# Kernel optimization log

Measured on AMD Instinct MI355X. Metric: run time of the kernel, lower is better.

## Reference

```python
import jax, jax.numpy as jnp
import numpy as np

DIM, ATT, G, T, KL, B = 1024, 128, 8, 4096, 256, 8
GD = DIM // G
SCALE = 1.0 / np.sqrt(ATT)

def setup_inputs() -> dict:
    key = jax.random.key(0)
    ks = jax.random.split(key, 7)
    x = jax.random.normal(ks[0], (B, T, DIM), dtype=jnp.float32)
    # stacked per-group weights (einsum orientation: in_dim x out_dim)
    Wq = jax.random.normal(ks[1], (G, GD, ATT), dtype=jnp.float32) * (1.0 / np.sqrt(GD))
    Wk = jax.random.normal(ks[2], (G, GD, ATT), dtype=jnp.float32) * (1.0 / np.sqrt(GD))
    Wv = jax.random.normal(ks[3], (G, GD, GD), dtype=jnp.float32) * (1.0 / np.sqrt(GD))
    Wo = jax.random.normal(ks[4], (G, GD, GD), dtype=jnp.float32) * (1.0 / np.sqrt(GD))
    Pk = jax.random.normal(ks[5], (G, T, KL), dtype=jnp.float32) * (1.0 / np.sqrt(T))
    Pv = jax.random.normal(ks[6], (G, T, KL), dtype=jnp.float32) * (1.0 / np.sqrt(T))
    return {"x": x, "Wq": Wq, "Wk": Wk, "Wv": Wv, "Wo": Wo, "Pk": Pk, "Pv": Pv}

def reference(x, Wq, Wk, Wv, Wo, Pk, Pv):
    Bx, Tx, _ = x.shape
    xg = x.reshape(Bx, Tx, G, GD).transpose(0, 2, 1, 3)        # [B,G,T,gd]
    q = jnp.einsum('bgtd,gda->bgta', xg, Wq)                   # [B,G,T,att]
    k = jnp.einsum('bgtd,gda->bgta', xg, Wk)
    v = jnp.einsum('bgtd,gde->bgte', xg, Wv)                   # [B,G,T,gd]
    k_red = jnp.einsum('bgta,gtk->bgka', k, Pk)                # [B,G,kl,att]
    v_red = jnp.einsum('bgte,gtk->bgke', v, Pv)                # [B,G,kl,gd]
    att = jax.nn.softmax(jnp.einsum('bgta,bgka->bgtk', q, k_red) * SCALE, axis=-1)
    out = jnp.einsum('bgtk,bgke->bgte', att, v_red)            # [B,G,T,gd]
    out = jnp.einsum('bgte,gef->bgtf', out, Wo)                # per-group output proj
    return out.transpose(0, 2, 1, 3).reshape(Bx, Tx, DIM)      # concat groups on last dim
```

## Files before the change

kernel.cpp:

```cpp
#include <hip/hip_runtime.h>
#include <hip/hip_bf16.h>

#define NB 8
#define NG 8
#define NT 4096
#define NDIM 1024
#define NGD 128
#define NATT 128
#define NKL 256
#define FSCALE 0.08838834764831845f

typedef __bf16 bf16x8 __attribute__((ext_vector_type(8)));
typedef float f32x4 __attribute__((ext_vector_type(4)));
typedef ushort u16x8 __attribute__((ext_vector_type(8)));
typedef ushort u16x4 __attribute__((ext_vector_type(4)));

#define MFMA(a, b, c) __builtin_amdgcn_mfma_f32_16x16x32_bf16(a, b, c, 0, 0, 0)

__device__ __forceinline__ ushort f2bf(float f) {
  union { float f; unsigned u; } v; v.f = f;
  unsigned r = v.u + 0x7FFFu + ((v.u >> 16) & 1u);
  return (ushort)(r >> 16);
}

__device__ __forceinline__ void gload16(const ushort* g, ushort* l) {
  __builtin_amdgcn_global_load_lds(
      (const __attribute__((address_space(1))) unsigned int*)g,
      (__attribute__((address_space(3))) unsigned int*)l, 16, 0, 0);
}

__global__ __launch_bounds__(512) void k0_weights(
    const float* __restrict__ Wq, const float* __restrict__ Wk,
    const float* __restrict__ Wv, const float* __restrict__ Wo,
    ushort* __restrict__ WkQT, ushort* __restrict__ WvoT) {
  const int sel = blockIdx.x;
  const int g = blockIdx.y;
  __shared__ float A2[128 * 136];
  __shared__ float B2[128 * 136];
  const int tid = threadIdx.x;

  if (sel == 0) {
#pragma unroll
    for (int u = 0; u < 8; ++u) {
      const int c = tid + 512 * u;
      const int row = c >> 5, c4 = (c & 31) * 4;
      *(float4*)&A2[row * 136 + c4] =
          *(const float4*)&Wo[(size_t)g * 16384 + row * 128 + c4];
      const float4 v = *(const float4*)&Wv[(size_t)g * 16384 + row * 128 + c4];
      B2[(c4 + 0) * 136 + row] = v.x;
      B2[(c4 + 1) * 136 + row] = v.y;
      B2[(c4 + 2) * 136 + row] = v.z;
      B2[(c4 + 3) * 136 + row] = v.w;
    }
  } else {
#pragma unroll
    for (int u = 0; u < 8; ++u) {
      const int c = tid + 512 * u;
      const int row = c >> 5, c4 = (c & 31) * 4;
      const float4 q = *(const float4*)&Wq[(size_t)g * 16384 + row * 128 + c4];
      A2[(c4 + 0) * 136 + row] = q.x;
      A2[(c4 + 1) * 136 + row] = q.y;
      A2[(c4 + 2) * 136 + row] = q.z;
      A2[(c4 + 3) * 136 + row] = q.w;
      const float4 k = *(const float4*)&Wk[(size_t)g * 16384 + row * 128 + c4];
      B2[(c4 + 0) * 136 + row] = k.x;
      B2[(c4 + 1) * 136 + row] = k.y;
      B2[(c4 + 2) * 136 + row] = k.z;
      B2[(c4 + 3) * 136 + row] = k.w;
    }
  }
  __syncthreads();

  const int mr = tid >> 4;
  const int mc = tid & 15;
  float acc[4][8];
#pragma unroll
  for (int i = 0; i < 4; ++i)
#pragma unroll
    for (int j = 0; j < 8; ++j) acc[i][j] = 0.f;

#pragma unroll 4
  for (int k = 0; k < 128; ++k) {
    const float4 a = *(const float4*)&A2[k * 136 + mr * 4];
    const float4 b0 = *(const float4*)&B2[k * 136 + mc * 8];
    const float4 b1 = *(const float4*)&B2[k * 136 + mc * 8 + 4];
    const float av[4] = {a.x, a.y, a.z, a.w};
    const float bv[8] = {b0.x, b0.y, b0.z, b0.w, b1.x, b1.y, b1.z, b1.w};
#pragma unroll
    for (int i = 0; i < 4; ++i)
#pragma unroll
      for (int j = 0; j < 8; ++j) acc[i][j] += av[i] * bv[j];
  }

  const float sc = sel ? FSCALE : 1.f;
  ushort* dst = (sel ? WkQT : WvoT) + (size_t)g * 16384;
#pragma unroll
  for (int i = 0; i < 4; ++i) {
    u16x8 pk;
#pragma unroll
    for (int j = 0; j < 8; ++j) pk[j] = f2bf(acc[i][j] * sc);
    *(u16x8*)&dst[(size_t)(mr * 4 + i) * 128 + mc * 8] = pk;
  }
}

__global__ __launch_bounds__(256) void kt_x(const float* __restrict__ x,
                                            ushort* __restrict__ xT) {
  const int t0 = blockIdx.x * 64;
  const int bg = blockIdx.y;
  const int b = bg >> 3, g = bg & 7;
  __shared__ float xl[64 * 132];
#pragma unroll
  for (int u = 0; u < 8; ++u) {
    const int c = threadIdx.x + 256 * u;
    const int row = c >> 5, c4 = (c & 31) * 4;
    *(float4*)&xl[row * 132 + c4] =
        *(const float4*)&x[((size_t)b * NT + t0 + row) * NDIM + g * 128 + c4];
  }
  __syncthreads();
  const int d = threadIdx.x >> 1, th = (threadIdx.x & 1) * 32;
  ushort* dst = xT + ((size_t)bg * 128 + d) * NT + t0 + th;
#pragma unroll
  for (int k = 0; k < 8; ++k) {
    u16x4 pk;
#pragma unroll
    for (int z = 0; z < 4; ++z) pk[z] = f2bf(xl[(th + k * 4 + z) * 132 + d]);
    *(u16x4*)&dst[k * 4] = pk;
  }
}

__global__ __launch_bounds__(256) void kt_p(const float* __restrict__ P,
                                            ushort* __restrict__ PT) {
  const int t0 = blockIdx.x * 64;
  const int klh = blockIdx.y, g = blockIdx.z;
  __shared__ float pl[64 * 132];
#pragma unroll
  for (int u = 0; u < 8; ++u) {
    const int c = threadIdx.x + 256 * u;
    const int row = c >> 5, c4 = (c & 31) * 4;
    *(float4*)&pl[row * 132 + c4] =
        *(const float4*)&P[((size_t)g * NT + t0 + row) * NKL + klh * 128 + c4];
  }
  __syncthreads();
  const int d = threadIdx.x >> 1, th = (threadIdx.x & 1) * 32;
  ushort* dst = PT + ((size_t)g * NKL + klh * 128 + d) * NT + t0 + th;
#pragma unroll
  for (int k = 0; k < 8; ++k) {
    u16x4 pk;
#pragma unroll
    for (int z = 0; z < 4; ++z) pk[z] = f2bf(pl[(th + k * 4 + z) * 132 + d]);
    *(u16x4*)&dst[k * 4] = pk;
  }
}

__global__ __launch_bounds__(256, 2) void k1_mfma(
    const ushort* __restrict__ PkT, const ushort* __restrict__ PvT,
    const ushort* __restrict__ xT, const ushort* __restrict__ WkQT,
    const ushort* __restrict__ WvoT, ushort* __restrict__ MQ,
    ushort* __restrict__ vo_redT) {
  const int klt = blockIdx.x;
  const int sel = blockIdx.y;
  const int bg = blockIdx.z;
  const int g = bg & 7;
  const ushort* PT = (sel ? PvT : PkT) + ((size_t)g * NKL + klt * 128) * NT;
  const ushort* Xb = xT + (size_t)bg * 128 * NT;

  __shared__ ushort lds[17408];

  const int tid = threadIdx.x;
  const int w = tid >> 6, lane = tid & 63;
  const int l15 = lane & 15, l4 = lane >> 4;
  const int rh = (w & 1) * 64;
  const int ch = (w >> 1) * 64;
  const int srow = lane >> 2, sc = lane & 3;

  f32x4 acc[4][4];
  const f32x4 fz = {0.f, 0.f, 0.f, 0.f};
#pragma unroll
  for (int i = 0; i < 4; ++i)
#pragma unroll
    for (int j = 0; j < 4; ++j) acc[i][j] = fz;

#define K1_STAGE(buf, s)                                                     \
  {                                                                          \
    const int t0_ = (s) * 32;                                                \
    ushort* Ab_ = &lds[(buf) * 8192];                                        \
    ushort* Bb_ = &lds[(buf) * 8192 + 4096];                                 \
    _Pragma("unroll") for (int u = 0; u < 2; ++u) {                          \
      const int row_ = w * 32 + u * 16 + srow;                               \
      const size_t off_ = (size_t)row_ * NT + t0_ + ((sc ^ (row_ & 3)) << 3);\
      gload16(PT + off_, Ab_ + (w * 32 + u * 16) * 32);                      \
      gload16(Xb + off_, Bb_ + (w * 32 + u * 16) * 32);                      \
    }                                                                        \
  }

#define K1_COMPUTE(buf)                                                      \
  {                                                                          \
    const ushort* Ab_ = &lds[(buf) * 8192];                                  \
    const ushort* Bb_ = &lds[(buf) * 8192 + 4096];                           \
    bf16x8 af_[4], bf_[4];                                                   \
    _Pragma("unroll") for (int i = 0; i < 4; ++i) {                          \
      const int row_ = rh + i * 16 + l15;                                    \
      af_[i] = *(const bf16x8*)&Ab_[row_ * 32 + ((l4 ^ (row_ & 3)) << 3)];   \
    }                                                                        \
    _Pragma("unroll") for (int j = 0; j < 4; ++j) {                          \
      const int row_ = ch + j * 16 + l15;                                    \
      bf_[j] = *(const bf16x8*)&Bb_[row_ * 32 + ((l4 ^ (row_ & 3)) << 3)];   \
    }                                                                        \
    _Pragma("unroll") for (int i = 0; i < 4; ++i)                            \
      _Pragma("unroll") for (int j = 0; j < 4; ++j)                          \
        acc[i][j] = MFMA(af_[i], bf_[j], acc[i][j]);                         \
  }

  K1_STAGE(0, 0);
  __syncthreads();
  int buf = 0;
#pragma unroll 1
  for (int s = 0; s < 128; ++s) {
    if (s + 1 < 128) K1_STAGE(buf ^ 1, s + 1);
    K1_COMPUTE(buf);
    __syncthreads();
    buf ^= 1;
  }

  ushort* C = lds;
#pragma unroll
  for (int i = 0; i < 4; ++i)
#pragma unroll
    for (int j = 0; j < 4; ++j)
#pragma unroll
      for (int r = 0; r < 4; ++r)
        C[(rh + i * 16 + l4 * 4 + r) * 136 + ch + j * 16 + l15] =
            f2bf(acc[i][j][r]);
  __syncthreads();

  const ushort* WT = (sel ? WvoT : WkQT) + (size_t)g * 16384;
  f32x4 o[4][4];
#pragma unroll
  for (int i = 0; i < 4; ++i)
#pragma unroll
    for (int j = 0; j < 4; ++j) o[i][j] = fz;
#pragma unroll
  for (int ks = 0; ks < 4; ++ks) {
    bf16x8 af[4], bfr[4];
#pragma unroll
    for (int i = 0; i < 4; ++i)
      af[i] = *(const bf16x8*)&C[(rh + i * 16 + l15) * 136 + ks * 32 + l4 * 8];
#pragma unroll
    for (int j = 0; j < 4; ++j)
      bfr[j] = *(const bf16x8*)&WT[(size_t)(ch + j * 16 + l15) * 128 + ks * 32 + l4 * 8];
#pragma unroll
    for (int i = 0; i < 4; ++i)
#pragma unroll
      for (int j = 0; j < 4; ++j) o[i][j] = MFMA(af[i], bfr[j], o[i][j]);
  }

  if (sel == 0) {
#pragma unroll
    for (int i = 0; i < 4; ++i)
#pragma unroll
      for (int j = 0; j < 4; ++j)
#pragma unroll
        for (int r = 0; r < 4; ++r)
          MQ[((size_t)bg * NKL + klt * 128 + rh + i * 16 + l4 * 4 + r) * 128 +
             ch + j * 16 + l15] = f2bf(o[i][j][r]);
  } else {
#pragma unroll
    for (int i = 0; i < 4; ++i)
#pragma unroll
      for (int j = 0; j < 4; ++j) {
        u16x4 pk;
#pragma unroll
        for (int r = 0; r < 4; ++r) pk[r] = f2bf(o[i][j][r]);
        *(u16x4*)&vo_redT[((size_t)bg * 128 + ch + j * 16 + l15) * NKL +
                          klt * 128 + rh + i * 16 + l4 * 4] = pk;
      }
  }
}

__global__ __launch_bounds__(512, 2) void k2_attn(
    const float* __restrict__ x, const ushort* __restrict__ MQ,
    const ushort* __restrict__ vo_redT, float* __restrict__ out) {
  const int tc = blockIdx.x;
  const int bg = blockIdx.y;
  const int b = bg >> 3, g = bg & 7;

  __shared__ ushort mq[256 * 136];
  __shared__ ushort att[64 * 264];
  __shared__ float redm[2][64];
  __shared__ float reds[2][64];

  const int tid = threadIdx.x;
  const int w = tid >> 6, lane = tid & 63;
  const int l15 = lane & 15, l4 = lane >> 4;
  const int tw = w >> 1, half = w & 1;
  const f32x4 fz = {0.f, 0.f, 0.f, 0.f};

  {
    const ushort* src = MQ + (size_t)bg * NKL * 128;
#pragma unroll
    for (int u = 0; u < 8; ++u) {
      const int c = tid + 512 * u;
      const int r = c >> 4, c8 = (c & 15) * 8;
      *(u16x8*)&mq[r * 136 + c8] = *(const u16x8*)&src[r * 128 + c8];
    }
  }

  const float* xb = x + ((size_t)b * NT + tc * 512) * NDIM + g * 128;
  const ushort* vo = vo_redT + ((size_t)bg * 128 + half * 64) * NKL;

  float4 xr[8];
#pragma unroll
  for (int ks = 0; ks < 4; ++ks) {
    const float* p = xb + (size_t)(tw * 16 + l15) * NDIM + ks * 32 + l4 * 8;
    xr[ks * 2] = *(const float4*)p;
    xr[ks * 2 + 1] = *(const float4*)(p + 4);
  }
  __syncthreads();

#pragma unroll 1
  for (int st = 0; st < 8; ++st) {
    bf16x8 a[4];
#pragma unroll
    for (int ks = 0; ks < 4; ++ks) {
      bf16x8 t;
      t[0] = (__bf16)xr[ks * 2].x; t[1] = (__bf16)xr[ks * 2].y;
      t[2] = (__bf16)xr[ks * 2].z; t[3] = (__bf16)xr[ks * 2].w;
      t[4] = (__bf16)xr[ks * 2 + 1].x; t[5] = (__bf16)xr[ks * 2 + 1].y;
      t[6] = (__bf16)xr[ks * 2 + 1].z; t[7] = (__bf16)xr[ks * 2 + 1].w;
      a[ks] = t;
    }
    if (st + 1 < 8) {
      const float* pn = xb + (size_t)((st + 1) * 64 + tw * 16 + l15) * NDIM;
#pragma unroll
      for (int ks = 0; ks < 4; ++ks) {
        xr[ks * 2] = *(const float4*)(pn + ks * 32 + l4 * 8);
        xr[ks * 2 + 1] = *(const float4*)(pn + ks * 32 + l4 * 8 + 4);
      }
    }
    f32x4 s[8];
#pragma unroll
    for (int n = 0; n < 8; ++n) s[n] = fz;
#pragma unroll
    for (int n = 0; n < 8; ++n) {
      const int row = (half * 8 + n) * 16 + l15;
#pragma unroll
      for (int ks = 0; ks < 4; ++ks) {
        const bf16x8 bv = *(const bf16x8*)&mq[row * 136 + ks * 32 + l4 * 8];
        s[n] = MFMA(a[ks], bv, s[n]);
      }
    }
    const int rowbase = tw * 16 + l4 * 4;
    float inv[4];
    {
      float mx[4];
#pragma unroll
      for (int r = 0; r < 4; ++r) {
        float m = s[0][r];
#pragma unroll
        for (int n = 1; n < 8; ++n) m = fmaxf(m, s[n][r]);
#pragma unroll
        for (int off = 1; off < 16; off <<= 1) m = fmaxf(m, __shfl_xor(m, off, 64));
        mx[r] = m;
      }
      if (l15 == 0) {
#pragma unroll
        for (int r = 0; r < 4; ++r) redm[half][rowbase + r] = mx[r];
      }
      __syncthreads();
      float sm[4];
#pragma unroll
      for (int r = 0; r < 4; ++r) {
        const float mg = fmaxf(mx[r], redm[half ^ 1][rowbase + r]);
        float acc = 0.f;
#pragma unroll
        for (int n = 0; n < 8; ++n) {
          const float p = __expf(s[n][r] - mg);
          acc += p;
          att[(rowbase + r) * 264 + (half * 8 + n) * 16 + l15] = f2bf(p);
        }
#pragma unroll
        for (int off = 1; off < 16; off <<= 1) acc += __shfl_xor(acc, off, 64);
        sm[r] = acc;
      }
      if (l15 == 0) {
#pragma unroll
        for (int r = 0; r < 4; ++r) reds[half][rowbase + r] = sm[r];
      }
      __syncthreads();
#pragma unroll
      for (int r = 0; r < 4; ++r)
        inv[r] = 1.f / (sm[r] + reds[half ^ 1][rowbase + r]);
    }
    f32x4 oa[4];
#pragma unroll
    for (int j = 0; j < 4; ++j) oa[j] = fz;
#pragma unroll
    for (int ks = 0; ks < 8; ++ks) {
      const bf16x8 av = *(const bf16x8*)&att[(tw * 16 + l15) * 264 + ks * 32 + l4 * 8];
#pragma unroll
      for (int j = 0; j < 4; ++j) {
        const bf16x8 bv = *(const bf16x8*)&vo[(size_t)(j * 16 + l15) * NKL + ks * 32 + l4 * 8];
        oa[j] = MFMA(av, bv, oa[j]);
      }
    }
    float* ob = out + ((size_t)b * NT + tc * 512 + st * 64 + tw * 16) * NDIM +
                g * 128 + half * 64;
#pragma unroll
    for (int j = 0; j < 4; ++j)
#pragma unroll
      for (int r = 0; r < 4; ++r)
        ob[(size_t)(l4 * 4 + r) * NDIM + j * 16 + l15] = oa[j][r] * inv[r];
  }
}

extern "C" void kernel_launch(void* const* d_in, const int* in_sizes, int n_in,
                              void* d_out, int out_size, void* d_ws, size_t ws_size,
                              hipStream_t stream) {
  (void)in_sizes; (void)n_in; (void)out_size; (void)ws_size;
  const float* x  = (const float*)d_in[0];
  const float* Wq = (const float*)d_in[1];
  const float* Wk = (const float*)d_in[2];
  const float* Wv = (const float*)d_in[3];
  const float* Wo = (const float*)d_in[4];
  const float* Pk = (const float*)d_in[5];
  const float* Pv = (const float*)d_in[6];

  ushort* wsu = (ushort*)d_ws;
  ushort* PkT     = wsu;
  ushort* PvT     = PkT + 8388608;
  ushort* WkQT    = PvT + 8388608;
  ushort* WvoT    = WkQT + 131072;
  ushort* MQ      = WvoT + 131072;
  ushort* vo_redT = MQ + 2097152;
  ushort* xT = (ushort*)d_out;

  k0_weights<<<dim3(2, NG), dim3(512), 0, stream>>>(Wq, Wk, Wv, Wo, WkQT, WvoT);
  kt_x<<<dim3(64, 64), dim3(256), 0, stream>>>(x, xT);
  kt_p<<<dim3(64, 2, 8), dim3(256), 0, stream>>>(Pk, PkT);
  kt_p<<<dim3(64, 2, 8), dim3(256), 0, stream>>>(Pv, PvT);
  k1_mfma<<<dim3(2, 2, 64), dim3(256), 0, stream>>>(PkT, PvT, xT, WkQT, WvoT,
                                                    MQ, vo_redT);
  k2_attn<<<dim3(8, 64), dim3(512), 0, stream>>>(x, MQ, vo_redT, (float*)d_out);
}
```

Measured before the change: 281.1 us.

## Restructure attention kernel to per-wave full rows, widen transposes, remap k1 blocks

```diff
diff --git a/kernel.cpp b/kernel.cpp
--- a/kernel.cpp
+++ b/kernel.cpp
@@ -117,14 +117,15 @@
         *(const float4*)&x[((size_t)b * NT + t0 + row) * NDIM + g * 128 + c4];
   }
   __syncthreads();
-  const int d = threadIdx.x >> 1, th = (threadIdx.x & 1) * 32;
-  ushort* dst = xT + ((size_t)bg * 128 + d) * NT + t0 + th;
-#pragma unroll
-  for (int k = 0; k < 8; ++k) {
-    u16x4 pk;
-#pragma unroll
-    for (int z = 0; z < 4; ++z) pk[z] = f2bf(xl[(th + k * 4 + z) * 132 + d]);
-    *(u16x4*)&dst[k * 4] = pk;
+  const int seg = threadIdx.x & 7;
+  const int d0 = threadIdx.x >> 3;
+#pragma unroll
+  for (int u = 0; u < 4; ++u) {
+    const int d = d0 + u * 32;
+    u16x8 pk;
+#pragma unroll
+    for (int z = 0; z < 8; ++z) pk[z] = f2bf(xl[(seg * 8 + z) * 132 + d]);
+    *(u16x8*)&xT[((size_t)bg * 128 + d) * NT + t0 + seg * 8] = pk;
   }
 }
 
@@ -141,14 +142,15 @@
         *(const float4*)&P[((size_t)g * NT + t0 + row) * NKL + klh * 128 + c4];
   }
   __syncthreads();
-  const int d = threadIdx.x >> 1, th = (threadIdx.x & 1) * 32;
-  ushort* dst = PT + ((size_t)g * NKL + klh * 128 + d) * NT + t0 + th;
-#pragma unroll
-  for (int k = 0; k < 8; ++k) {
-    u16x4 pk;
-#pragma unroll
-    for (int z = 0; z < 4; ++z) pk[z] = f2bf(pl[(th + k * 4 + z) * 132 + d]);
-    *(u16x4*)&dst[k * 4] = pk;
+  const int seg = threadIdx.x & 7;
+  const int k0 = threadIdx.x >> 3;
+#pragma unroll
+  for (int u = 0; u < 4; ++u) {
+    const int kl = k0 + u * 32;
+    u16x8 pk;
+#pragma unroll
+    for (int z = 0; z < 8; ++z) pk[z] = f2bf(pl[(seg * 8 + z) * 132 + kl]);
+    *(u16x8*)&PT[((size_t)g * NKL + klh * 128 + kl) * NT + t0 + seg * 8] = pk;
   }
 }
 
@@ -157,9 +159,11 @@
     const ushort* __restrict__ xT, const ushort* __restrict__ WkQT,
     const ushort* __restrict__ WvoT, ushort* __restrict__ MQ,
     ushort* __restrict__ vo_redT) {
-  const int klt = blockIdx.x;
-  const int sel = blockIdx.y;
-  const int bg = blockIdx.z;
+  const int bid = blockIdx.x;
+  const int work = (bid & 7) * 32 + (bid >> 3);
+  const int bg = work >> 2;
+  const int sel = (work >> 1) & 1;
+  const int klt = work & 1;
   const int g = bg & 7;
   const ushort* PT = (sel ? PvT : PkT) + ((size_t)g * NKL + klt * 128) * NT;
   const ushort* Xb = xT + (size_t)bg * 128 * NT;
@@ -277,7 +281,7 @@
   }
 }
 
-__global__ __launch_bounds__(512, 2) void k2_attn(
+__global__ __launch_bounds__(512) void k2_attn(
     const float* __restrict__ x, const ushort* __restrict__ MQ,
     const ushort* __restrict__ vo_redT, float* __restrict__ out) {
   const int tc = blockIdx.x;
@@ -285,15 +289,26 @@
   const int b = bg >> 3, g = bg & 7;
 
   __shared__ ushort mq[256 * 136];
-  __shared__ ushort att[64 * 264];
-  __shared__ float redm[2][64];
-  __shared__ float reds[2][64];
+  __shared__ ushort att[8 * 16 * 272];
 
   const int tid = threadIdx.x;
   const int w = tid >> 6, lane = tid & 63;
   const int l15 = lane & 15, l4 = lane >> 4;
-  const int tw = w >> 1, half = w & 1;
+  ushort* attw = att + w * 16 * 272;
   const f32x4 fz = {0.f, 0.f, 0.f, 0.f};
+
+  const float* xb = x + ((size_t)b * NT + tc * 1024) * NDIM + g * 128;
+  const ushort* vo = vo_redT + (size_t)bg * 128 * NKL;
+
+  float4 xr[16];
+#pragma unroll
+  for (int rt = 0; rt < 2; ++rt)
+#pragma unroll
+    for (int ks = 0; ks < 4; ++ks) {
+      const float* p = xb + (size_t)(w * 32 + rt * 16 + l15) * NDIM + ks * 32 + l4 * 8;
+      xr[rt * 8 + ks * 2] = *(const float4*)p;
+      xr[rt * 8 + ks * 2 + 1] = *(const float4*)(p + 4);
+    }
 
   {
     const ushort* src = MQ + (size_t)bg * NKL * 128;
@@ -304,112 +319,138 @@
       *(u16x8*)&mq[r * 136 + c8] = *(const u16x8*)&src[r * 128 + c8];
     }
   }
-
-  const float* xb = x + ((size_t)b * NT + tc * 512) * NDIM + g * 128;
-  const ushort* vo = vo_redT + ((size_t)bg * 128 + half * 64) * NKL;
-
-  float4 xr[8];
-#pragma unroll
-  for (int ks = 0; ks < 4; ++ks) {
-    const float* p = xb + (size_t)(tw * 16 + l15) * NDIM + ks * 32 + l4 * 8;
-    xr[ks * 2] = *(const float4*)p;
-    xr[ks * 2 + 1] = *(const float4*)(p + 4);
-  }
   __syncthreads();
 
 #pragma unroll 1
-  for (int st = 0; st < 8; ++st) {
-    bf16x8 a[4];
+  for (int st = 0; st < 4; ++st) {
+    bf16x8 a0[4], a1[4];
 #pragma unroll
     for (int ks = 0; ks < 4; ++ks) {
-      bf16x8 t;
-      t[0] = (__bf16)xr[ks * 2].x; t[1] = (__bf16)xr[ks * 2].y;
-      t[2] = (__bf16)xr[ks * 2].z; t[3] = (__bf16)xr[ks * 2].w;
-      t[4] = (__bf16)xr[ks * 2 + 1].x; t[5] = (__bf16)xr[ks * 2 + 1].y;
-      t[6] = (__bf16)xr[ks * 2 + 1].z; t[7] = (__bf16)xr[ks * 2 + 1].w;
-      a[ks] = t;
-    }
-    if (st + 1 < 8) {
-      const float* pn = xb + (size_t)((st + 1) * 64 + tw * 16 + l15) * NDIM;
-#pragma unroll
-      for (int ks = 0; ks < 4; ++ks) {
-        xr[ks * 2] = *(const float4*)(pn + ks * 32 + l4 * 8);
-        xr[ks * 2 + 1] = *(const float4*)(pn + ks * 32 + l4 * 8 + 4);
+      bf16x8 t0, t1;
+      const float4 u0 = xr[ks * 2], u1 = xr[ks * 2 + 1];
+      const float4 v0 = xr[8 + ks * 2], v1 = xr[8 + ks * 2 + 1];
+      t0[0] = (__bf16)u0.x; t0[1] = (__bf16)u0.y; t0[2] = (__bf16)u0.z; t0[3] = (__bf16)u0.w;
+      t0[4] = (__bf16)u1.x; t0[5] = (__bf16)u1.y; t0[6] = (__bf16)u1.z; t0[7] = (__bf16)u1.w;
+      t1[0] = (__bf16)v0.x; t1[1] = (__bf16)v0.y; t1[2] = (__bf16)v0.z; t1[3] = (__bf16)v0.w;
+      t1[4] = (__bf16)v1.x; t1[5] = (__bf16)v1.y; t1[6] = (__bf16)v1.z; t1[7] = (__bf16)v1.w;
+      a0[ks] = t0; a1[ks] = t1;
+    }
+
+    f32x4 s0[16], s1[16];
+#pragma unroll
+    for (int n = 0; n < 16; ++n) { s0[n] = fz; s1[n] = fz; }
+#pragma unroll
+    for (int ks = 0; ks < 4; ++ks)
+#pragma unroll
+      for (int n = 0; n < 16; ++n) {
+        const bf16x8 mf = *(const bf16x8*)&mq[(n * 16 + l15) * 136 + ks * 32 + l4 * 8];
+        s0[n] = MFMA(mf, a0[ks], s0[n]);
+        s1[n] = MFMA(mf, a1[ks], s1[n]);
       }
-    }
-    f32x4 s[8];
-#pragma unroll
-    for (int n = 0; n < 8; ++n) s[n] = fz;
-#pragma unroll
-    for (int n = 0; n < 8; ++n) {
-      const int row = (half * 8 + n) * 16 + l15;
-#pragma unroll
-      for (int ks = 0; ks < 4; ++ks) {
-        const bf16x8 bv = *(const bf16x8*)&mq[row * 136 + ks * 32 + l4 * 8];
-        s[n] = MFMA(a[ks], bv, s[n]);
+
+    float inv0, inv1;
+    {
+      f32x4 m4 = s0[0];
+#pragma unroll
+      for (int n = 1; n < 16; ++n)
+#pragma unroll
+        for (int r = 0; r < 4; ++r) m4[r] = fmaxf(m4[r], s0[n][r]);
+      float m = fmaxf(fmaxf(m4[0], m4[1]), fmaxf(m4[2], m4[3]));
+      m = fmaxf(m, __shfl_xor(m, 16, 64));
+      m = fmaxf(m, __shfl_xor(m, 32, 64));
+      f32x4 sum4 = fz;
+#pragma unroll
+      for (int n = 0; n < 16; ++n)
+#pragma unroll
+        for (int r = 0; r < 4; ++r) {
+          const float p = __expf(s0[n][r] - m);
+          s0[n][r] = p;
+          sum4[r] += p;
+        }
+      float sm = (sum4[0] + sum4[1]) + (sum4[2] + sum4[3]);
+      sm += __shfl_xor(sm, 16, 64);
+      sm += __shfl_xor(sm, 32, 64);
+      inv0 = 1.f / sm;
+    }
+    {
+      f32x4 m4 = s1[0];
+#pragma unroll
+      for (int n = 1; n < 16; ++n)
+#pragma unroll
+        for (int r = 0; r < 4; ++r) m4[r] = fmaxf(m4[r], s1[n][r]);
+      float m = fmaxf(fmaxf(m4[0], m4[1]), fmaxf(m4[2], m4[3]));
+      m = fmaxf(m, __shfl_xor(m, 16, 64));
+      m = fmaxf(m, __shfl_xor(m, 32, 64));
+      f32x4 sum4 = fz;
+#pragma unroll
+      for (int n = 0; n < 16; ++n)
+#pragma unroll
+        for (int r = 0; r < 4; ++r) {
+          const float p = __expf(s1[n][r] - m);
+          s1[n][r] = p;
+          sum4[r] += p;
+        }
+      float sm = (sum4[0] + sum4[1]) + (sum4[2] + sum4[3]);
+      sm += __shfl_xor(sm, 16, 64);
+      sm += __shfl_xor(sm, 32, 64);
+      inv1 = 1.f / sm;
+    }
+
+    bf16x8 attf0[8], attf1[8];
+#pragma unroll
+    for (int n = 0; n < 16; ++n) {
+      u16x4 pk;
+#pragma unroll
+      for (int r = 0; r < 4; ++r) pk[r] = f2bf(s0[n][r] * inv0);
+      *(u16x4*)&attw[l15 * 272 + n * 16 + l4 * 4] = pk;
+    }
+#pragma unroll
+    for (int ks = 0; ks < 8; ++ks)
+      attf0[ks] = *(const bf16x8*)&attw[l15 * 272 + ks * 32 + l4 * 8];
+#pragma unroll
+    for (int n = 0; n < 16; ++n) {
+      u16x4 pk;
+#pragma unroll
+      for (int r = 0; r < 4; ++r) pk[r] = f2bf(s1[n][r] * inv1);
+      *(u16x4*)&attw[l15 * 272 + n * 16 + l4 * 4] = pk;
+    }
+#pragma unroll
+    for (int ks = 0; ks < 8; ++ks)
+      attf1[ks] = *(const bf16x8*)&attw[l15 * 272 + ks * 32 + l4 * 8];
+
+    if (st < 3) {
+      const float* pn = xb + (size_t)((st + 1) * 256 + w * 32) * NDIM;
+#pragma unroll
+      for (int rt = 0; rt < 2; ++rt)
+#pragma unroll
+        for (int ks = 0; ks < 4; ++ks) {
+          const float* p = pn + (size_t)(rt * 16 + l15) * NDIM + ks * 32 + l4 * 8;
+          xr[rt * 8 + ks * 2] = *(const float4*)p;
+          xr[rt * 8 + ks * 2 + 1] = *(const float4*)(p + 4);
+        }
+    }
+
+    f32x4 oa0[8], oa1[8];
+#pragma unroll
+    for (int dt = 0; dt < 8; ++dt) { oa0[dt] = fz; oa1[dt] = fz; }
+#pragma unroll
+    for (int ks = 0; ks < 8; ++ks)
+#pragma unroll
+      for (int dt = 0; dt < 8; ++dt) {
+        const bf16x8 vf =
+            *(const bf16x8*)&vo[(size_t)(dt * 16 + l15) * NKL + ks * 32 + l4 * 8];
+        oa0[dt] = MFMA(attf0[ks], vf, oa0[dt]);
+        oa1[dt] = MFMA(attf1[ks], vf, oa1[dt]);
       }
-    }
-    const int rowbase = tw * 16 + l4 * 4;
-    float inv[4];
-    {
-      float mx[4];
+
+    float* ob = out + ((size_t)b * NT + tc * 1024 + st * 256 + w * 32) * NDIM + g * 128;
+#pragma unroll
+    for (int dt = 0; dt < 8; ++dt)
 #pragma unroll
       for (int r = 0; r < 4; ++r) {
-        float m = s[0][r];
-#pragma unroll
-        for (int n = 1; n < 8; ++n) m = fmaxf(m, s[n][r]);
-#pragma unroll
-        for (int off = 1; off < 16; off <<= 1) m = fmaxf(m, __shfl_xor(m, off, 64));
-        mx[r] = m;
+        ob[(size_t)(l4 * 4 + r) * NDIM + dt * 16 + l15] = oa0[dt][r];
+        ob[(size_t)(16 + l4 * 4 + r) * NDIM + dt * 16 + l15] = oa1[dt][r];
       }
-      if (l15 == 0) {
-#pragma unroll
-        for (int r = 0; r < 4; ++r) redm[half][rowbase + r] = mx[r];
-      }
-      __syncthreads();
-      float sm[4];
-#pragma unroll
-      for (int r = 0; r < 4; ++r) {
-        const float mg = fmaxf(mx[r], redm[half ^ 1][rowbase + r]);
-        float acc = 0.f;
-#pragma unroll
-        for (int n = 0; n < 8; ++n) {
-          const float p = __expf(s[n][r] - mg);
-          acc += p;
-          att[(rowbase + r) * 264 + (half * 8 + n) * 16 + l15] = f2bf(p);
-        }
-#pragma unroll
-        for (int off = 1; off < 16; off <<= 1) acc += __shfl_xor(acc, off, 64);
-        sm[r] = acc;
-      }
-      if (l15 == 0) {
-#pragma unroll
-        for (int r = 0; r < 4; ++r) reds[half][rowbase + r] = sm[r];
-      }
-      __syncthreads();
-#pragma unroll
-      for (int r = 0; r < 4; ++r)
-        inv[r] = 1.f / (sm[r] + reds[half ^ 1][rowbase + r]);
-    }
-    f32x4 oa[4];
-#pragma unroll
-    for (int j = 0; j < 4; ++j) oa[j] = fz;
-#pragma unroll
-    for (int ks = 0; ks < 8; ++ks) {
-      const bf16x8 av = *(const bf16x8*)&att[(tw * 16 + l15) * 264 + ks * 32 + l4 * 8];
-#pragma unroll
-      for (int j = 0; j < 4; ++j) {
-        const bf16x8 bv = *(const bf16x8*)&vo[(size_t)(j * 16 + l15) * NKL + ks * 32 + l4 * 8];
-        oa[j] = MFMA(av, bv, oa[j]);
-      }
-    }
-    float* ob = out + ((size_t)b * NT + tc * 512 + st * 64 + tw * 16) * NDIM +
-                g * 128 + half * 64;
-#pragma unroll
-    for (int j = 0; j < 4; ++j)
-#pragma unroll
-      for (int r = 0; r < 4; ++r)
-        ob[(size_t)(l4 * 4 + r) * NDIM + j * 16 + l15] = oa[j][r] * inv[r];
   }
 }
 
@@ -438,7 +479,7 @@
   kt_x<<<dim3(64, 64), dim3(256), 0, stream>>>(x, xT);
   kt_p<<<dim3(64, 2, 8), dim3(256), 0, stream>>>(Pk, PkT);
   kt_p<<<dim3(64, 2, 8), dim3(256), 0, stream>>>(Pv, PvT);
-  k1_mfma<<<dim3(2, 2, 64), dim3(256), 0, stream>>>(PkT, PvT, xT, WkQT, WvoT,
-                                                    MQ, vo_redT);
-  k2_attn<<<dim3(8, 64), dim3(512), 0, stream>>>(x, MQ, vo_redT, (float*)d_out);
-}
+  k1_mfma<<<dim3(256), dim3(256), 0, stream>>>(PkT, PvT, xT, WkQT, WvoT,
+                                               MQ, vo_redT);
+  k2_attn<<<dim3(4, 64), dim3(512), 0, stream>>>(x, MQ, vo_redT, (float*)d_out);
+}
```

New measurement: 561.3 us. 99.7% more time.
